# Performance work log

Measured on AMD Instinct MI355X. Metric: run time of the kernel, lower is better.

## Reference

```python
import jax, jax.numpy as jnp
import numpy as np

N_NODES = 20000
N_EDGES = 320000
D_IN = 128
D_OUT = 128
HEADS = 12
BN_EPS = 1e-5


def setup_inputs() -> dict:
    key = jax.random.key(0)
    ks = jax.random.split(key, 24)
    x = jax.random.normal(ks[0], (N_NODES, D_IN), dtype=jnp.float32)
    # edges guaranteed to have no self loops (so remove_self_loops is a no-op)
    src = jax.random.randint(ks[1], (N_EDGES,), 0, N_NODES, dtype=jnp.int32)
    off = jax.random.randint(ks[2], (N_EDGES,), 1, N_NODES, dtype=jnp.int32)
    dst = (src + off) % N_NODES
    edge_index = jnp.stack([src, dst], axis=0)
    inp = {"x": x, "edge_index": edge_index}
    # per-layer FeatureSteeredConvolution params (torch init: uniform weights, N(0,0.1) c/bias)
    dims_in = [D_IN, D_OUT, D_OUT]
    k = 3
    for li in range(3):
        din = dims_in[li]
        inp[f"l{li}_Wlin"] = jax.random.uniform(ks[k], (HEADS * D_OUT, din), dtype=jnp.float32); k += 1
        inp[f"l{li}_Wu"] = jax.random.uniform(ks[k], (HEADS, din), dtype=jnp.float32); k += 1
        inp[f"l{li}_c"] = 0.1 * jax.random.normal(ks[k], (HEADS,), dtype=jnp.float32); k += 1
        inp[f"l{li}_b"] = 0.1 * jax.random.normal(ks[k], (D_OUT,), dtype=jnp.float32); k += 1
    for bi in range(2):
        inp[f"bn{bi}_g"] = jnp.ones((D_OUT,), dtype=jnp.float32)
        inp[f"bn{bi}_b"] = jnp.zeros((D_OUT,), dtype=jnp.float32)
    return inp


def _fsc(x, src, dst, Wlin, Wu, c, b):
    """FeatureSteeredConvolution: edge gather -> softmax attention over heads ->
    per-head linear -> scatter-mean over destination nodes."""
    n = x.shape[0]
    x_j = x[src]                                  # [E, Cin] source features
    x_i = x[dst]                                  # [E, Cin] target features
    att = jax.nn.softmax((x_i - x_j) @ Wu.T + c, axis=1)   # [E, H]
    Wl = Wlin.reshape(HEADS, D_OUT, -1)           # [H, Cout, Cin]
    msg = jnp.zeros((src.shape[0], D_OUT), dtype=x.dtype)
    for h in range(HEADS):                        # small fixed loop over heads
        msg = msg + att[:, h:h + 1] * (x_j @ Wl[h].T)
    agg = jax.ops.segment_sum(msg, dst, num_segments=n)
    deg = jax.ops.segment_sum(jnp.ones((dst.shape[0],), dtype=x.dtype), dst, num_segments=n)
    return agg / jnp.maximum(deg, 1.0)[:, None] + b


def _bn(x, g, b):
    # BatchNorm1d in training mode: biased batch statistics
    m = jnp.mean(x, axis=0)
    v = jnp.var(x, axis=0)
    return (x - m) * jax.lax.rsqrt(v + BN_EPS) * g + b


def reference(x, edge_index, l0_Wlin, l0_Wu, l0_c, l0_b, bn0_g, bn0_b,
              l1_Wlin, l1_Wu, l1_c, l1_b, bn1_g, bn1_b,
              l2_Wlin, l2_Wu, l2_c, l2_b):
    n = x.shape[0]
    loops = jnp.arange(n, dtype=edge_index.dtype)
    src = jnp.concatenate([edge_index[0], loops])
    dst = jnp.concatenate([edge_index[1], loops])
    h = jax.nn.relu(_fsc(x, src, dst, l0_Wlin, l0_Wu, l0_c, l0_b))
    h = _bn(h, bn0_g, bn0_b)
    h = jax.nn.relu(_fsc(h, src, dst, l1_Wlin, l1_Wu, l1_c, l1_b))
    h = _bn(h, bn1_g, bn1_b)
    return _fsc(h, src, dst, l2_Wlin, l2_Wu, l2_c, l2_b)
```

## Files before the change

kernel.cpp:

```cpp
#include <hip/hip_runtime.h>
#include <hip/hip_bf16.h>

#define DHID 128
#define NH 12
#define KDIM 1536
#define KSPLIT 3
#define KSL (KDIM / KSPLIT)
#define BK 64
#define NCHUNK (KSL / BK)
#define COMBB 512

typedef __attribute__((ext_vector_type(8))) short short8;
typedef __attribute__((ext_vector_type(4))) float f32x4;

static __device__ __forceinline__ unsigned short f2bf(float f) {
  __hip_bfloat16 h = __float2bfloat16(f);
  return __builtin_bit_cast(unsigned short, h);
}
static __device__ __forceinline__ float bf2f(unsigned short u) {
  unsigned v = ((unsigned)u) << 16;
  return __builtin_bit_cast(float, v);
}
static __device__ __forceinline__ float rfl_f(float x) {
  return __builtin_bit_cast(float, __builtin_amdgcn_readfirstlane(__builtin_bit_cast(int, x)));
}
static __device__ __forceinline__ void gload_lds16(const void* g, void* l) {
  __builtin_amdgcn_global_load_lds(
      (const __attribute__((address_space(1))) unsigned int*)g,
      (__attribute__((address_space(3))) unsigned int*)l, 16, 0, 0);
}


__global__ void hist_k(const int* __restrict__ dstp, int* __restrict__ cnt, int e0, int et) {
  int e = blockIdx.x * blockDim.x + threadIdx.x;
  if (e >= et) return;
  int d = (e < e0) ? dstp[e] : (e - e0);
  atomicAdd(&cnt[d], 1);
}

__global__ void scan_k(const int* __restrict__ cnt, int* __restrict__ row_start,
                       int* __restrict__ cursor, int n, int total) {
  __shared__ int part[1024];
  int t = threadIdx.x;
  const int CH = (n + 1023) >> 10;
  int base = t * CH;
  int s = 0;
  for (int j = 0; j < CH; ++j) { int i = base + j; if (i < n) s += cnt[i]; }
  part[t] = s;
  __syncthreads();
  for (int off = 1; off < 1024; off <<= 1) {
    int v = (t >= off) ? part[t - off] : 0;
    __syncthreads();
    part[t] += v;
    __syncthreads();
  }
  int run = (t == 0) ? 0 : part[t - 1];
  for (int j = 0; j < CH; ++j) {
    int i = base + j;
    if (i < n) {
      int c = cnt[i];
      row_start[i] = run;
      cursor[i] = run;
      run += c;
    }
  }
  if (t == 0) row_start[n] = total;
}

__global__ void scatter_k(const int* __restrict__ srcp, const int* __restrict__ dstp,
                          int* __restrict__ cursor, int* __restrict__ srcs,
                          int* __restrict__ dsts, int e0, int et) {
  int e = blockIdx.x * blockDim.x + threadIdx.x;
  if (e >= et) return;
  int s = (e < e0) ? srcp[e] : (e - e0);
  int d = (e < e0) ? dstp[e] : (e - e0);
  int pos = atomicAdd(&cursor[d], 1);
  srcs[pos] = s;
  dsts[pos] = d;
}


template<int BN>
__global__ void u_k(const float* __restrict__ in, const float* __restrict__ Wu,
                    const float* __restrict__ sc, const float* __restrict__ sh,
                    unsigned short* __restrict__ xb, float* __restrict__ u, int n) {
  int wid = (blockIdx.x * blockDim.x + threadIdx.x) >> 6;
  if (wid >= n) return;
  int lane = threadIdx.x & 63;
  float2 xv = *(const float2*)(in + (long)wid * DHID + 2 * lane);
  if (BN) {
    float2 scv = *(const float2*)(sc + 2 * lane);
    float2 shv = *(const float2*)(sh + 2 * lane);
    xv.x = xv.x * scv.x + shv.x;
    xv.y = xv.y * scv.y + shv.y;
  }
  unsigned pv = (unsigned)f2bf(xv.x) | ((unsigned)f2bf(xv.y) << 16);
  *(unsigned*)(xb + (long)wid * DHID + 2 * lane) = pv;
  #pragma unroll
  for (int h = 0; h < NH; ++h) {
    float2 wv = *(const float2*)(Wu + h * DHID + 2 * lane);
    float p = xv.x * wv.x + xv.y * wv.y;
    p += __shfl_xor(p, 1);  p += __shfl_xor(p, 2);  p += __shfl_xor(p, 4);
    p += __shfl_xor(p, 8);  p += __shfl_xor(p, 16); p += __shfl_xor(p, 32);
    if (lane == 0) u[wid * NH + h] = p;
  }
}


__global__ void att_k(const float* __restrict__ u, const float* __restrict__ cvec,
                      const int* __restrict__ srcs, const int* __restrict__ dsts,
                      const int* __restrict__ row_start, float* __restrict__ attS, int et) {
  int j = blockIdx.x * blockDim.x + threadIdx.x;
  if (j >= et) return;
  int s = srcs[j], d = dsts[j];
  const float4* ud = (const float4*)(u + (long)d * NH);
  const float4* us = (const float4*)(u + (long)s * NH);
  const float4* cp = (const float4*)cvec;
  float w[NH];
  #pragma unroll
  for (int q = 0; q < 3; ++q) {
    float4 a = ud[q], b = us[q], c = cp[q];
    w[4*q+0] = a.x - b.x + c.x;
    w[4*q+1] = a.y - b.y + c.y;
    w[4*q+2] = a.z - b.z + c.z;
    w[4*q+3] = a.w - b.w + c.w;
  }
  float m = w[0];
  #pragma unroll
  for (int h = 1; h < NH; ++h) m = fmaxf(m, w[h]);
  float ssum = 0.f;
  #pragma unroll
  for (int h = 0; h < NH; ++h) { w[h] = __expf(w[h] - m); ssum += w[h]; }
  float deg = (float)(row_start[d + 1] - row_start[d]);
  float inv = 1.f / (ssum * deg);
  float4* op = (float4*)(attS + (long)j * NH);
  #pragma unroll
  for (int q = 0; q < 3; ++q) {
    float4 v;
    v.x = w[4*q+0] * inv; v.y = w[4*q+1] * inv;
    v.z = w[4*q+2] * inv; v.w = w[4*q+3] * inv;
    op[q] = v;
  }
}


__global__ void edge_k(const unsigned short* __restrict__ xb, const float* __restrict__ attS,
                       const int* __restrict__ srcs, const int* __restrict__ row_start,
                       unsigned short* __restrict__ A, int n) {
  int wid = __builtin_amdgcn_readfirstlane((int)((blockIdx.x * blockDim.x + threadIdx.x) >> 6));
  if (wid >= n) return;
  int lane = threadIdx.x & 63;
  float acc[NH][2];
  #pragma unroll
  for (int h = 0; h < NH; ++h) { acc[h][0] = 0.f; acc[h][1] = 0.f; }
  int beg = __builtin_amdgcn_readfirstlane(row_start[wid]);
  int end = __builtin_amdgcn_readfirstlane(row_start[wid + 1]);
  int j = beg;
  for (; j + 7 < end; j += 8) {
    int sx[8];
    #pragma unroll
    for (int i = 0; i < 8; ++i)
      sx[i] = __builtin_amdgcn_readfirstlane(srcs[j + i]);
    unsigned pv[8];
    #pragma unroll
    for (int i = 0; i < 8; ++i)
      pv[i] = *(const unsigned*)(xb + (long)sx[i] * DHID + 2 * lane);
    #pragma unroll
    for (int i = 0; i < 8; ++i) {
      const float* ap = attS + (long)(j + i) * NH;
      float xv0 = bf2f((unsigned short)pv[i]);
      float xv1 = bf2f((unsigned short)(pv[i] >> 16));
      #pragma unroll
      for (int h = 0; h < NH; ++h) {
        float a = rfl_f(ap[h]);
        acc[h][0] += a * xv0;
        acc[h][1] += a * xv1;
      }
    }
  }
  for (; j < end; ++j) {
    int s0 = __builtin_amdgcn_readfirstlane(srcs[j]);
    unsigned pv = *(const unsigned*)(xb + (long)s0 * DHID + 2 * lane);
    float xv0 = bf2f((unsigned short)pv);
    float xv1 = bf2f((unsigned short)(pv >> 16));
    const float* ap = attS + (long)j * NH;
    #pragma unroll
    for (int h = 0; h < NH; ++h) {
      float a = rfl_f(ap[h]);
      acc[h][0] += a * xv0;
      acc[h][1] += a * xv1;
    }
  }
  unsigned* Ap = (unsigned*)(A + (long)wid * KDIM);
  #pragma unroll
  for (int h = 0; h < NH; ++h) {
    unsigned pv = (unsigned)f2bf(acc[h][0]) | ((unsigned)f2bf(acc[h][1]) << 16);
    Ap[h * (DHID / 2) + lane] = pv;
  }
}


__global__ void prep_wcat_k(const float* __restrict__ W0, const float* __restrict__ W1,
                            const float* __restrict__ W2, unsigned short* __restrict__ Wcat3) {
  int t = blockIdx.x * blockDim.x + threadIdx.x;
  int l = t / (DHID * KDIM), r = t - l * (DHID * KDIM);
  int c = r / KDIM, f = r - c * KDIM;
  int h = f >> 7, k = f & (DHID - 1);
  const float* W = (l == 0) ? W0 : (l == 1) ? W1 : W2;
  Wcat3[t] = f2bf(W[((h << 7) + c) * DHID + k]);
}


__global__ __launch_bounds__(256) void gemm_k(
    const unsigned short* __restrict__ A, const unsigned short* __restrict__ B,
    float* __restrict__ part, float* __restrict__ outp, int M) {
  __shared__ __align__(16) char smem[2 * 24576];
  int w = threadIdx.x >> 6, lane = threadIdx.x & 63;
  int lr = lane & 15, lq = lane >> 4;
  int m0 = blockIdx.x * 64, n0 = w * 32;
  int ks = blockIdx.y;
  const long kbeg = (long)ks * KSL;
  f32x4 acc[4][2];
  #pragma unroll
  for (int mf = 0; mf < 4; ++mf)
    #pragma unroll
    for (int nf = 0; nf < 2; ++nf) acc[mf][nf] = (f32x4){0.f, 0.f, 0.f, 0.f};
  const char* Ag = (const char*)A;
  const char* Bg = (const char*)B;

  auto stage = [&](int c, int p) {
    const long kpos = kbeg + (long)c * BK;
    #pragma unroll
    for (int jj = 0; jj < 2; ++jj) {
      int L = w * 2048 + jj * 1024 + lane * 16;
      int r = L >> 7;
      int srcin = (L & 127) ^ ((r & 7) << 4);
      const char* g = Ag + ((long)(m0 + r) * KDIM + kpos) * 2 + srcin;
      gload_lds16(g, &smem[p * 24576 + w * 2048 + jj * 1024]);
    }
    #pragma unroll
    for (int jj = 0; jj < 4; ++jj) {
      int L = w * 4096 + jj * 1024 + lane * 16;
      int r = L >> 7;
      int srcin = (L & 127) ^ ((r & 7) << 4);
      const char* g = Bg + ((long)r * KDIM + kpos) * 2 + srcin;
      gload_lds16(g, &smem[p * 24576 + 8192 + w * 4096 + jj * 1024]);
    }
  };

  auto compute = [&](int p) {
    const char* Ab = &smem[p * 24576];
    const char* Bb = &smem[p * 24576 + 8192];
    #pragma unroll
    for (int kst = 0; kst < 2; ++kst) {
      short8 av[4], bv[2];
      #pragma unroll
      for (int mf = 0; mf < 4; ++mf) {
        int row = mf * 16 + lr;
        int off = row * 128 + ((kst * 64 + lq * 16) ^ ((row & 7) << 4));
        av[mf] = *(const short8*)(Ab + off);
      }
      #pragma unroll
      for (int nf = 0; nf < 2; ++nf) {
        int row = n0 + nf * 16 + lr;
        int off = row * 128 + ((kst * 64 + lq * 16) ^ ((row & 7) << 4));
        bv[nf] = *(const short8*)(Bb + off);
      }
      #pragma unroll
      for (int mf = 0; mf < 4; ++mf)
        #pragma unroll
        for (int nf = 0; nf < 2; ++nf)
          acc[mf][nf] = __builtin_amdgcn_mfma_f32_16x16x32_bf16(av[mf], bv[nf], acc[mf][nf], 0, 0, 0);
    }
  };

  stage(0, 0);
  for (int c = 0; c < NCHUNK; ++c) {
    if (c + 1 < NCHUNK) {
      stage(c + 1, (c + 1) & 1);
      asm volatile("s_waitcnt vmcnt(6)" ::: "memory");
    } else {
      asm volatile("s_waitcnt vmcnt(0)" ::: "memory");
    }
    __syncthreads();
    compute(c & 1);
    __syncthreads();
  }

  float* op = (ks == 0) ? outp : (part + (long)(ks - 1) * M * DHID);
  #pragma unroll
  for (int mf = 0; mf < 4; ++mf) {
    #pragma unroll
    for (int nf = 0; nf < 2; ++nf) {
      int c = n0 + nf * 16 + lr;
      int rowb = m0 + mf * 16 + lq * 4;
      #pragma unroll
      for (int r = 0; r < 4; ++r) {
        int row = rowb + r;
        if (row < M) op[(long)row * DHID + c] = acc[mf][nf][r];
      }
    }
  }
}


template<int RELU, int DOBN>
__global__ __launch_bounds__(256) void combine_k(
    const float* __restrict__ part, const float* __restrict__ bias,
    float* __restrict__ outp, float* __restrict__ bnpart, int M) {
  const int nvec = M * (DHID / 4);
  const int stride = COMBB * 256;
  int t0 = blockIdx.x * 256 + threadIdx.x;
  int c = (t0 & 31) * 4;
  float4 bc = *(const float4*)(bias + c);
  float s0=0,s1=0,s2=0,s3=0,q0=0,q1=0,q2=0,q3=0;
  for (int t = t0; t < nvec; t += stride) {
    long idx = (long)t * 4;
    float4 v  = *(const float4*)(outp + idx);
    float4 p1 = *(const float4*)(part + idx);
    float4 p2 = *(const float4*)(part + (long)M * DHID + idx);
    v.x += p1.x + p2.x + bc.x;
    v.y += p1.y + p2.y + bc.y;
    v.z += p1.z + p2.z + bc.z;
    v.w += p1.w + p2.w + bc.w;
    if (RELU) {
      v.x = fmaxf(v.x, 0.f); v.y = fmaxf(v.y, 0.f);
      v.z = fmaxf(v.z, 0.f); v.w = fmaxf(v.w, 0.f);
    }
    *(float4*)(outp + idx) = v;
    if (DOBN) {
      s0 += v.x; s1 += v.y; s2 += v.z; s3 += v.w;
      q0 += v.x*v.x; q1 += v.y*v.y; q2 += v.z*v.z; q3 += v.w*v.w;
    }
  }
  if (DOBN) {
    s0 += __shfl_xor(s0, 32); s1 += __shfl_xor(s1, 32);
    s2 += __shfl_xor(s2, 32); s3 += __shfl_xor(s3, 32);
    q0 += __shfl_xor(q0, 32); q1 += __shfl_xor(q1, 32);
    q2 += __shfl_xor(q2, 32); q3 += __shfl_xor(q3, 32);
    __shared__ float red[4][256];
    int w = threadIdx.x >> 6, lane = threadIdx.x & 63;
    if (lane < 32) {
      int cb = lane * 4;
      red[w][cb+0] = s0; red[w][cb+1] = s1; red[w][cb+2] = s2; red[w][cb+3] = s3;
      red[w][128+cb+0] = q0; red[w][128+cb+1] = q1; red[w][128+cb+2] = q2; red[w][128+cb+3] = q3;
    }
    __syncthreads();
    int tt = threadIdx.x;
    bnpart[blockIdx.x * 256 + tt] = red[0][tt] + red[1][tt] + red[2][tt] + red[3][tt];
  }
}


__global__ void bnfin_k(const float* __restrict__ bnpart,
                        const float* __restrict__ g, const float* __restrict__ b,
                        float* __restrict__ sc, float* __restrict__ sh, float invn) {
  __shared__ float col[256];
  int t = threadIdx.x;
  float s = 0.f;
  #pragma unroll 8
  for (int bb = 0; bb < COMBB; ++bb) s += bnpart[bb * 256 + t];
  col[t] = s;
  __syncthreads();
  if (t < DHID) {
    float m = col[t] * invn;
    float v = col[128 + t] * invn - m * m;
    float rs = rsqrtf(v + 1e-5f);
    float sg = g[t] * rs;
    sc[t] = sg;
    sh[t] = b[t] - m * sg;
  }
}


extern "C" void kernel_launch(void* const* d_in, const int* in_sizes, int n_in,
                              void* d_out, int out_size, void* d_ws, size_t ws_size,
                              hipStream_t stream) {
  const float* x = (const float*)d_in[0];
  const int* ei = (const int*)d_in[1];
  const int N = in_sizes[0] / DHID;
  const int E0 = in_sizes[1] / 2;
  const int ET = E0 + N;
  const int* srcp = ei;
  const int* dstp = ei + E0;
  const float* Wlin[3] = {(const float*)d_in[2], (const float*)d_in[6], (const float*)d_in[10]};
  const float* Wu[3]   = {(const float*)d_in[3], (const float*)d_in[7], (const float*)d_in[11]};
  const float* cc[3]   = {(const float*)d_in[4], (const float*)d_in[8], (const float*)d_in[12]};
  const float* bb[3]   = {(const float*)d_in[5], (const float*)d_in[9], (const float*)d_in[13]};
  const float* bng[2]  = {(const float*)d_in[14], (const float*)d_in[16]};
  const float* bnb[2]  = {(const float*)d_in[15], (const float*)d_in[17]};

  const int MPAD = ((N + 63) / 64) * 64;

  size_t o = 0;
  char* base = (char*)d_ws;
  auto carve = [&](size_t bytes) -> char* {
    char* p = base + o;
    o += (bytes + 255) & ~(size_t)255;
    return p;
  };
  int* row_start = (int*)carve((size_t)(N + 1) * 4);
  int* cursor    = (int*)carve((size_t)N * 4);
  int* srcs      = (int*)carve((size_t)ET * 4);
  int* dsts      = (int*)carve((size_t)ET * 4);
  float* u       = (float*)carve((size_t)N * NH * 4);
  float* bnpart  = (float*)carve((size_t)COMBB * 256 * 4);
  float* bnsc    = (float*)carve((size_t)DHID * 4);
  float* bnsh    = (float*)carve((size_t)DHID * 4);
  unsigned short* Wcat3 = (unsigned short*)carve((size_t)3 * DHID * KDIM * 2);
  float* hA      = (float*)carve((size_t)N * DHID * 4);
  unsigned short* xb = (unsigned short*)carve((size_t)N * DHID * 2);
  unsigned short* A  = (unsigned short*)carve((size_t)MPAD * KDIM * 2);
  size_t attS_bytes = (size_t)ET * NH * 4;
  size_t part_bytes = (size_t)(KSPLIT - 1) * N * DHID * 4;
  char* shared_rg = carve(attS_bytes > part_bytes ? attS_bytes : part_bytes);
  float* attS = (float*)shared_rg;
  float* partb = (float*)shared_rg;
  (void)ws_size; (void)n_in; (void)out_size;

  const int EB = (ET + 255) / 256;
  const int NW = (N + 3) / 4;
  const int MB64 = (N + 63) / 64;

  hipMemsetAsync(cursor, 0, (size_t)N * 4, stream);
  hist_k<<<EB, 256, 0, stream>>>(dstp, cursor, E0, ET);
  scan_k<<<1, 1024, 0, stream>>>(cursor, row_start, cursor, N, ET);
  scatter_k<<<EB, 256, 0, stream>>>(srcp, dstp, cursor, srcs, dsts, E0, ET);
  prep_wcat_k<<<(3 * DHID * KDIM) / 256, 256, 0, stream>>>(Wlin[0], Wlin[1], Wlin[2], Wcat3);

  for (int li = 0; li < 3; ++li) {
    const bool last = (li == 2);
    if (li == 0) u_k<0><<<NW, 256, 0, stream>>>(x, Wu[0], bnsc, bnsh, xb, u, N);
    else         u_k<1><<<NW, 256, 0, stream>>>(hA, Wu[li], bnsc, bnsh, xb, u, N);
    att_k<<<EB, 256, 0, stream>>>(u, cc[li], srcs, dsts, row_start, attS, ET);
    edge_k<<<NW, 256, 0, stream>>>(xb, attS, srcs, row_start, A, N);
    float* outp = last ? (float*)d_out : hA;
    gemm_k<<<dim3(MB64, KSPLIT), 256, 0, stream>>>(A, Wcat3 + (size_t)li * DHID * KDIM, partb, outp, N);
    if (!last) {
      combine_k<1, 1><<<COMBB, 256, 0, stream>>>(partb, bb[li], outp, bnpart, N);
      bnfin_k<<<1, 256, 0, stream>>>(bnpart, bng[li], bnb[li], bnsc, bnsh, 1.f / (float)N);
    } else {
      combine_k<0, 0><<<COMBB, 256, 0, stream>>>(partb, bb[li], outp, bnpart, N);
    }
  }
}
```

Before: 481.1 us.

## Fuse attention softmax into edge aggregation kernel via per-wave LDS staging

```diff
diff --git a/kernel.cpp b/kernel.cpp
--- a/kernel.cpp
+++ b/kernel.cpp
@@ -20,9 +20,6 @@
 static __device__ __forceinline__ float bf2f(unsigned short u) {
   unsigned v = ((unsigned)u) << 16;
   return __builtin_bit_cast(float, v);
-}
-static __device__ __forceinline__ float rfl_f(float x) {
-  return __builtin_bit_cast(float, __builtin_amdgcn_readfirstlane(__builtin_bit_cast(int, x)));
 }
 static __device__ __forceinline__ void gload_lds16(const void* g, void* l) {
   __builtin_amdgcn_global_load_lds(
@@ -107,89 +104,103 @@
 }
 
 
-__global__ void att_k(const float* __restrict__ u, const float* __restrict__ cvec,
-                      const int* __restrict__ srcs, const int* __restrict__ dsts,
-                      const int* __restrict__ row_start, float* __restrict__ attS, int et) {
-  int j = blockIdx.x * blockDim.x + threadIdx.x;
-  if (j >= et) return;
-  int s = srcs[j], d = dsts[j];
-  const float4* ud = (const float4*)(u + (long)d * NH);
-  const float4* us = (const float4*)(u + (long)s * NH);
-  const float4* cp = (const float4*)cvec;
-  float w[NH];
-  #pragma unroll
-  for (int q = 0; q < 3; ++q) {
-    float4 a = ud[q], b = us[q], c = cp[q];
-    w[4*q+0] = a.x - b.x + c.x;
-    w[4*q+1] = a.y - b.y + c.y;
-    w[4*q+2] = a.z - b.z + c.z;
-    w[4*q+3] = a.w - b.w + c.w;
-  }
-  float m = w[0];
-  #pragma unroll
-  for (int h = 1; h < NH; ++h) m = fmaxf(m, w[h]);
-  float ssum = 0.f;
-  #pragma unroll
-  for (int h = 0; h < NH; ++h) { w[h] = __expf(w[h] - m); ssum += w[h]; }
-  float deg = (float)(row_start[d + 1] - row_start[d]);
-  float inv = 1.f / (ssum * deg);
-  float4* op = (float4*)(attS + (long)j * NH);
-  #pragma unroll
-  for (int q = 0; q < 3; ++q) {
-    float4 v;
-    v.x = w[4*q+0] * inv; v.y = w[4*q+1] * inv;
-    v.z = w[4*q+2] * inv; v.w = w[4*q+3] * inv;
-    op[q] = v;
-  }
-}
-
-
-__global__ void edge_k(const unsigned short* __restrict__ xb, const float* __restrict__ attS,
-                       const int* __restrict__ srcs, const int* __restrict__ row_start,
-                       unsigned short* __restrict__ A, int n) {
-  int wid = __builtin_amdgcn_readfirstlane((int)((blockIdx.x * blockDim.x + threadIdx.x) >> 6));
+__global__ void edge_k(const unsigned short* __restrict__ xb, const float* __restrict__ u,
+                       const float* __restrict__ cvec, const int* __restrict__ srcs,
+                       const int* __restrict__ row_start, unsigned short* __restrict__ A, int n) {
+  __shared__ float attL[4][64][NH];
+  int w4 = threadIdx.x >> 6;
+  int wid = __builtin_amdgcn_readfirstlane((int)(blockIdx.x * 4 + w4));
   if (wid >= n) return;
   int lane = threadIdx.x & 63;
+  int beg = __builtin_amdgcn_readfirstlane(row_start[wid]);
+  int end = __builtin_amdgcn_readfirstlane(row_start[wid + 1]);
+  float invdeg = 1.f / (float)(end - beg);
+  float uic[NH];
+  {
+    const float4* up = (const float4*)(u + (long)wid * NH);
+    const float4* cp = (const float4*)cvec;
+    #pragma unroll
+    for (int q = 0; q < 3; ++q) {
+      float4 a = up[q], c = cp[q];
+      uic[4*q+0] = a.x + c.x; uic[4*q+1] = a.y + c.y;
+      uic[4*q+2] = a.z + c.z; uic[4*q+3] = a.w + c.w;
+    }
+  }
   float acc[NH][2];
   #pragma unroll
   for (int h = 0; h < NH; ++h) { acc[h][0] = 0.f; acc[h][1] = 0.f; }
-  int beg = __builtin_amdgcn_readfirstlane(row_start[wid]);
-  int end = __builtin_amdgcn_readfirstlane(row_start[wid + 1]);
-  int j = beg;
-  for (; j + 7 < end; j += 8) {
-    int sx[8];
-    #pragma unroll
-    for (int i = 0; i < 8; ++i)
-      sx[i] = __builtin_amdgcn_readfirstlane(srcs[j + i]);
-    unsigned pv[8];
-    #pragma unroll
-    for (int i = 0; i < 8; ++i)
-      pv[i] = *(const unsigned*)(xb + (long)sx[i] * DHID + 2 * lane);
-    #pragma unroll
-    for (int i = 0; i < 8; ++i) {
-      const float* ap = attS + (long)(j + i) * NH;
-      float xv0 = bf2f((unsigned short)pv[i]);
-      float xv1 = bf2f((unsigned short)(pv[i] >> 16));
+
+  for (int c0 = beg; c0 < end; c0 += 64) {
+    int m = end - c0; if (m > 64) m = 64;
+    if (lane < m) {
+      int s = srcs[c0 + lane];
+      const float4* usp = (const float4*)(u + (long)s * NH);
+      float4 u0 = usp[0], u1 = usp[1], u2 = usp[2];
+      float wv[NH];
+      wv[0]=uic[0]-u0.x; wv[1]=uic[1]-u0.y; wv[2] =uic[2]-u0.z;  wv[3] =uic[3]-u0.w;
+      wv[4]=uic[4]-u1.x; wv[5]=uic[5]-u1.y; wv[6] =uic[6]-u1.z;  wv[7] =uic[7]-u1.w;
+      wv[8]=uic[8]-u2.x; wv[9]=uic[9]-u2.y; wv[10]=uic[10]-u2.z; wv[11]=uic[11]-u2.w;
+      float mx = wv[0];
+      #pragma unroll
+      for (int h = 1; h < NH; ++h) mx = fmaxf(mx, wv[h]);
+      float ssum = 0.f;
+      #pragma unroll
+      for (int h = 0; h < NH; ++h) { wv[h] = __expf(wv[h] - mx); ssum += wv[h]; }
+      float inv = invdeg / ssum;
+      float4* op = (float4*)attL[w4][lane];
+      float4 v0, v1, v2;
+      v0.x=wv[0]*inv;  v0.y=wv[1]*inv;  v0.z=wv[2]*inv;  v0.w=wv[3]*inv;
+      v1.x=wv[4]*inv;  v1.y=wv[5]*inv;  v1.z=wv[6]*inv;  v1.w=wv[7]*inv;
+      v2.x=wv[8]*inv;  v2.y=wv[9]*inv;  v2.z=wv[10]*inv; v2.w=wv[11]*inv;
+      op[0] = v0; op[1] = v1; op[2] = v2;
+    }
+    asm volatile("s_waitcnt lgkmcnt(0)" ::: "memory");
+    __builtin_amdgcn_wave_barrier();
+    int jj = 0;
+    for (; jj + 3 < m; jj += 4) {
+      int sx[4];
+      #pragma unroll
+      for (int i = 0; i < 4; ++i)
+        sx[i] = __builtin_amdgcn_readfirstlane(srcs[c0 + jj + i]);
+      unsigned pv[4];
+      #pragma unroll
+      for (int i = 0; i < 4; ++i)
+        pv[i] = *(const unsigned*)(xb + (long)sx[i] * DHID + 2 * lane);
+      #pragma unroll
+      for (int i = 0; i < 4; ++i) {
+        const float4* ap = (const float4*)attL[w4][jj + i];
+        float4 a0 = ap[0], a1 = ap[1], a2 = ap[2];
+        float xv0 = bf2f((unsigned short)pv[i]);
+        float xv1 = bf2f((unsigned short)(pv[i] >> 16));
+        float av[NH];
+        av[0]=a0.x; av[1]=a0.y; av[2] =a0.z; av[3] =a0.w;
+        av[4]=a1.x; av[5]=a1.y; av[6] =a1.z; av[7] =a1.w;
+        av[8]=a2.x; av[9]=a2.y; av[10]=a2.z; av[11]=a2.w;
+        #pragma unroll
+        for (int h = 0; h < NH; ++h) {
+          acc[h][0] += av[h] * xv0;
+          acc[h][1] += av[h] * xv1;
+        }
+      }
+    }
+    for (; jj < m; ++jj) {
+      int s0 = __builtin_amdgcn_readfirstlane(srcs[c0 + jj]);
+      unsigned pv = *(const unsigned*)(xb + (long)s0 * DHID + 2 * lane);
+      const float4* ap = (const float4*)attL[w4][jj];
+      float4 a0 = ap[0], a1 = ap[1], a2 = ap[2];
+      float xv0 = bf2f((unsigned short)pv);
+      float xv1 = bf2f((unsigned short)(pv >> 16));
+      float av[NH];
+      av[0]=a0.x; av[1]=a0.y; av[2] =a0.z; av[3] =a0.w;
+      av[4]=a1.x; av[5]=a1.y; av[6] =a1.z; av[7] =a1.w;
+      av[8]=a2.x; av[9]=a2.y; av[10]=a2.z; av[11]=a2.w;
       #pragma unroll
       for (int h = 0; h < NH; ++h) {
-        float a = rfl_f(ap[h]);
-        acc[h][0] += a * xv0;
-        acc[h][1] += a * xv1;
+        acc[h][0] += av[h] * xv0;
+        acc[h][1] += av[h] * xv1;
       }
     }
-  }
-  for (; j < end; ++j) {
-    int s0 = __builtin_amdgcn_readfirstlane(srcs[j]);
-    unsigned pv = *(const unsigned*)(xb + (long)s0 * DHID + 2 * lane);
-    float xv0 = bf2f((unsigned short)pv);
-    float xv1 = bf2f((unsigned short)(pv >> 16));
-    const float* ap = attS + (long)j * NH;
-    #pragma unroll
-    for (int h = 0; h < NH; ++h) {
-      float a = rfl_f(ap[h]);
-      acc[h][0] += a * xv0;
-      acc[h][1] += a * xv1;
-    }
+    __builtin_amdgcn_wave_barrier();
   }
   unsigned* Ap = (unsigned*)(A + (long)wid * KDIM);
   #pragma unroll
@@ -411,11 +422,7 @@
   float* hA      = (float*)carve((size_t)N * DHID * 4);
   unsigned short* xb = (unsigned short*)carve((size_t)N * DHID * 2);
   unsigned short* A  = (unsigned short*)carve((size_t)MPAD * KDIM * 2);
-  size_t attS_bytes = (size_t)ET * NH * 4;
-  size_t part_bytes = (size_t)(KSPLIT - 1) * N * DHID * 4;
-  char* shared_rg = carve(attS_bytes > part_bytes ? attS_bytes : part_bytes);
-  float* attS = (float*)shared_rg;
-  float* partb = (float*)shared_rg;
+  float* partb   = (float*)carve((size_t)(KSPLIT - 1) * N * DHID * 4);
   (void)ws_size; (void)n_in; (void)out_size;
 
   const int EB = (ET + 255) / 256;
@@ -432,8 +439,7 @@
     const bool last = (li == 2);
     if (li == 0) u_k<0><<<NW, 256, 0, stream>>>(x, Wu[0], bnsc, bnsh, xb, u, N);
     else         u_k<1><<<NW, 256, 0, stream>>>(hA, Wu[li], bnsc, bnsh, xb, u, N);
-    att_k<<<EB, 256, 0, stream>>>(u, cc[li], srcs, dsts, row_start, attS, ET);
-    edge_k<<<NW, 256, 0, stream>>>(xb, attS, srcs, row_start, A, N);
+    edge_k<<<NW, 256, 0, stream>>>(xb, u, cc[li], srcs, row_start, A, N);
     float* outp = last ? (float*)d_out : hA;
     gemm_k<<<dim3(MB64, KSPLIT), 256, 0, stream>>>(A, Wcat3 + (size_t)li * DHID * KDIM, partb, outp, N);
     if (!last) {
```

New measurement: 439.4 us. 1.1x faster.
